# Performance work log

Hardware: AMD Instinct MI355X
Metric: run time of the kernel (lower is better)

Reference implementation:

```python
import jax, jax.numpy as jnp
import numpy as np

B, N, D, H = 4, 2048, 512, 8
HD = D // H


def setup_inputs() -> dict:
    key = jax.random.key(0)
    ks = jax.random.split(key, 12)
    s = 1.0 / np.sqrt(D)
    return {
        "node_feat": jax.random.normal(ks[0], (B, N, D), jnp.float32),
        "edge_weights": jax.random.uniform(ks[1], (B, N, N), jnp.float32),
        "adj_matrix": jax.random.uniform(ks[2], (B, N, N), jnp.float32),
        "masks": jnp.ones((B, N), jnp.float32),
        "class_token": 0.02 * jax.random.normal(ks[3], (1, 1, D), jnp.float32),
        "Wq": jax.random.uniform(ks[4], (D, D), jnp.float32, -s, s),
        "bq": jnp.zeros((D,), jnp.float32),
        "Wk": jax.random.uniform(ks[5], (D, D), jnp.float32, -s, s),
        "bk": jnp.zeros((D,), jnp.float32),
        "Wv": jax.random.uniform(ks[6], (D, D), jnp.float32, -s, s),
        "bv": jnp.zeros((D,), jnp.float32),
        "Wo": jax.random.uniform(ks[7], (D, D), jnp.float32, -s, s),
        "bo": jnp.zeros((D,), jnp.float32),
        "gamma": jnp.ones((D,), jnp.float32),
        "beta": jnp.zeros((D,), jnp.float32),
    }


def _attn_mask(edge_weights, masks):
    # inner block: edge gates + self-loops, clamped at 1
    inner = jnp.minimum(edge_weights + jnp.eye(N, dtype=edge_weights.dtype), 1.0)
    top = jnp.concatenate([jnp.ones((B, 1, 1), edge_weights.dtype), masks[:, None, :]], axis=2)  # [B,1,1+N]
    bot = jnp.concatenate([jnp.ones((B, N, 1), edge_weights.dtype), inner], axis=2)              # [B,N,1+N]
    m = jnp.concatenate([top, bot], axis=1)  # [B,1+N,1+N]
    ext = jnp.concatenate([jnp.ones((B, 1), masks.dtype), masks], axis=1)  # [B,1+N], CLS always valid
    return m * ext[:, None, :] * ext[:, :, None]


def reference(node_feat, edge_weights, adj_matrix, masks, class_token,
              Wq, bq, Wk, bk, Wv, bv, Wo, bo, gamma, beta):
    x = jnp.concatenate([jnp.broadcast_to(class_token, (B, 1, D)), node_feat], axis=1)  # [B,1+N,D]
    S = 1 + N
    q = (x @ Wq.T + bq).reshape(B, S, H, HD).transpose(0, 2, 1, 3)
    k = (x @ Wk.T + bk).reshape(B, S, H, HD).transpose(0, 2, 1, 3)
    v = (x @ Wv.T + bv).reshape(B, S, H, HD).transpose(0, 2, 1, 3)
    scores = jnp.einsum('bhqd,bhkd->bhqk', q, k) / jnp.sqrt(jnp.float32(HD))
    m = _attn_mask(edge_weights, masks)
    scores = jnp.where(m[:, None, :, :] == 0, jnp.float32(-1e9), scores)
    attn = jax.nn.softmax(scores, axis=-1)
    out = jnp.einsum('bhqk,bhkd->bhqd', attn, v).transpose(0, 2, 1, 3).reshape(B, S, D)
    out = out @ Wo.T + bo
    y = out + x
    mu = jnp.mean(y, axis=-1, keepdims=True)
    var = jnp.mean((y - mu) ** 2, axis=-1, keepdims=True)
    y = (y - mu) / jnp.sqrt(var + 1e-5) * gamma + beta
    return y[:, 0, :]
```

## Files before the change

kernel.cpp:

```cpp
#include <hip/hip_runtime.h>

#define B_ 4
#define N_ 2048
#define D_ 512
#define H_ 8
#define S_ (N_ + 1)
#define NSLOT 132

#define Q0_OFF 0
#define TQ_OFF 1024
#define PW_OFF 8192
#define PZ_OFF (PW_OFF + NSLOT * B_ * H_ * D_)
#define W_OFF  (PZ_OFF + NSLOT * B_ * H_)
#define O0_OFF (W_OFF + B_ * H_ * D_)
#define Y_OFF  (O0_OFF + B_ * D_)

__device__ __forceinline__ float wave_reduce_sum(float v) {
    #pragma unroll
    for (int off = 32; off > 0; off >>= 1) v += __shfl_down(v, off, 64);
    return v;
}
__device__ __forceinline__ float wave_allreduce_sum(float v) {
    #pragma unroll
    for (int off = 1; off < 64; off <<= 1) v += __shfl_xor(v, off, 64);
    return v;
}

__global__ void q0_kernel(const float* __restrict__ ct,
                          const float* __restrict__ Wq, const float* __restrict__ bq,
                          float* __restrict__ ws) {
    int wv = threadIdx.x >> 6, lane = threadIdx.x & 63;
    int r = blockIdx.x * 8 + wv;
    const float4* c4 = (const float4*)ct;
    float4 ca = c4[lane * 2], cb = c4[lane * 2 + 1];
    const float4* row = (const float4*)(Wq + (size_t)r * D_);
    float4 a = row[lane * 2], b = row[lane * 2 + 1];
    float acc = a.x*ca.x + a.y*ca.y + a.z*ca.z + a.w*ca.w
              + b.x*cb.x + b.y*cb.y + b.z*cb.z + b.w*cb.w;
    acc = wave_reduce_sum(acc);
    if (lane == 0) ws[Q0_OFF + r] = acc + bq[r];
}

__global__ void tq_kernel(const float* __restrict__ Wk, float* __restrict__ ws) {
    int h = blockIdx.x, jc = blockIdx.y;
    int tid = threadIdx.x;
    __shared__ float q0s[64];
    if (tid < 64) q0s[tid] = ws[Q0_OFF + h * 64 + tid];
    __syncthreads();
    int j = jc * 128 + tid;
    float acc = 0.f;
    #pragma unroll 8
    for (int d2 = 0; d2 < 64; ++d2)
        acc += q0s[d2] * Wk[(size_t)(h * 64 + d2) * D_ + j];
    ws[TQ_OFF + h * D_ + j] = acc;
}

__global__ void fused_kernel(const float* __restrict__ nf, const float* __restrict__ ct,
                             const float* __restrict__ masks, float* __restrict__ ws) {
    int chunk = blockIdx.x, b = blockIdx.y;
    int wv = threadIdx.x >> 6, lane = threadIdx.x & 63;
    int slot = chunk * 4 + wv;
    int s0 = chunk * 64 + wv * 16;
    const float4* tq4 = (const float4*)(ws + TQ_OFF);
    float4 tqa[H_], tqb[H_];
    #pragma unroll
    for (int h = 0; h < H_; ++h) {
        tqa[h] = tq4[h * 128 + lane * 2];
        tqb[h] = tq4[h * 128 + lane * 2 + 1];
    }
    float4 acca[H_], accb[H_];
    float z[H_];
    #pragma unroll
    for (int h = 0; h < H_; ++h) {
        acca[h] = make_float4(0.f, 0.f, 0.f, 0.f);
        accb[h] = make_float4(0.f, 0.f, 0.f, 0.f);
        z[h] = 0.f;
    }
    for (int i = 0; i < 16; ++i) {
        int s = s0 + i;
        bool valid = (s < S_);
        const float* xrow = (!valid || s == 0) ? ct : (nf + ((size_t)b * N_ + (s - 1)) * D_);
        const float4* x4 = (const float4*)xrow;
        float4 xa = x4[lane * 2], xb = x4[lane * 2 + 1];
        float msk = 1.0f;
        if (valid && s > 0) msk = masks[b * N_ + s - 1];
        float gate = (valid && msk != 0.0f) ? 1.0f : 0.0f;
        float p[H_];
        #pragma unroll
        for (int h = 0; h < H_; ++h) {
            p[h] = tqa[h].x*xa.x + tqa[h].y*xa.y + tqa[h].z*xa.z + tqa[h].w*xa.w
                 + tqb[h].x*xb.x + tqb[h].y*xb.y + tqb[h].z*xb.z + tqb[h].w*xb.w;
            p[h] = wave_allreduce_sum(p[h]);
        }
        #pragma unroll
        for (int h = 0; h < H_; ++h) {
            float e = gate * __expf(p[h] * 0.125f);
            z[h] += e;
            acca[h].x += e * xa.x; acca[h].y += e * xa.y;
            acca[h].z += e * xa.z; acca[h].w += e * xa.w;
            accb[h].x += e * xb.x; accb[h].y += e * xb.y;
            accb[h].z += e * xb.z; accb[h].w += e * xb.w;
        }
    }
    float4* pw4 = (float4*)(ws + PW_OFF);
    size_t base = ((size_t)slot * B_ + b) * H_;
    #pragma unroll
    for (int h = 0; h < H_; ++h) {
        pw4[(base + h) * 128 + lane * 2]     = acca[h];
        pw4[(base + h) * 128 + lane * 2 + 1] = accb[h];
    }
    if (lane == 0) {
        #pragma unroll
        for (int h = 0; h < H_; ++h)
            ws[PZ_OFF + (slot * B_ + b) * H_ + h] = z[h];
    }
}

__global__ void reduce_w_kernel(float* __restrict__ ws) {
    int b = blockIdx.x / H_, h = blockIdx.x % H_;
    int tid = threadIdx.x;
    __shared__ float zl[128];
    float zp = 0.f;
    for (int slot = tid; slot < NSLOT; slot += 128)
        zp += ws[PZ_OFF + (slot * B_ + b) * H_ + h];
    zl[tid] = zp;
    __syncthreads();
    for (int st = 64; st > 0; st >>= 1) {
        if (tid < st) zl[tid] += zl[tid + st];
        __syncthreads();
    }
    float zinv = 1.0f / zl[0];
    const float4* pw4 = (const float4*)(ws + PW_OFF);
    float4 acc = make_float4(0.f, 0.f, 0.f, 0.f);
    #pragma unroll 4
    for (int slot = 0; slot < NSLOT; ++slot) {
        float4 v = pw4[(((size_t)slot * B_ + b) * H_ + h) * 128 + tid];
        acc.x += v.x; acc.y += v.y; acc.z += v.z; acc.w += v.w;
    }
    acc.x *= zinv; acc.y *= zinv; acc.z *= zinv; acc.w *= zinv;
    ((float4*)(ws + W_OFF))[(b * H_ + h) * 128 + tid] = acc;
}

__global__ void wv_kernel(const float* __restrict__ Wv, const float* __restrict__ bv,
                          float* __restrict__ ws) {
    int b = blockIdx.x;
    int wv = threadIdx.x >> 6, lane = threadIdx.x & 63;
    int r = blockIdx.y * 4 + wv;
    const float4* wrow = (const float4*)(ws + W_OFF + (size_t)b * H_ * D_ + (size_t)(r >> 6) * D_);
    float4 wa = wrow[lane * 2], wb = wrow[lane * 2 + 1];
    const float4* row = (const float4*)(Wv + (size_t)r * D_);
    float4 a = row[lane * 2], c = row[lane * 2 + 1];
    float acc = a.x*wa.x + a.y*wa.y + a.z*wa.z + a.w*wa.w
              + c.x*wb.x + c.y*wb.y + c.z*wb.z + c.w*wb.w;
    acc = wave_reduce_sum(acc);
    if (lane == 0) ws[O0_OFF + b * D_ + r] = acc + bv[r];
}

__global__ void wo_kernel(const float* __restrict__ Wo, const float* __restrict__ bo,
                          const float* __restrict__ ct, float* __restrict__ ws) {
    int b = blockIdx.x;
    int wv = threadIdx.x >> 6, lane = threadIdx.x & 63;
    int r = blockIdx.y * 4 + wv;
    const float4* ov = (const float4*)(ws + O0_OFF + (size_t)b * D_);
    float4 oa = ov[lane * 2], ob = ov[lane * 2 + 1];
    const float4* row = (const float4*)(Wo + (size_t)r * D_);
    float4 a = row[lane * 2], c = row[lane * 2 + 1];
    float acc = a.x*oa.x + a.y*oa.y + a.z*oa.z + a.w*oa.w
              + c.x*ob.x + c.y*ob.y + c.z*ob.z + c.w*ob.w;
    acc = wave_reduce_sum(acc);
    if (lane == 0) ws[Y_OFF + b * D_ + r] = acc + bo[r] + ct[r];
}

__global__ void ln_kernel(const float* __restrict__ gamma, const float* __restrict__ beta,
                          const float* __restrict__ ws, float* __restrict__ out) {
    int b = blockIdx.x;
    int tid = threadIdx.x, wv = tid >> 6, lane = tid & 63;
    float v = ws[Y_OFF + b * D_ + tid];
    float s1 = v, s2 = v * v;
    #pragma unroll
    for (int off = 32; off > 0; off >>= 1) {
        s1 += __shfl_down(s1, off, 64);
        s2 += __shfl_down(s2, off, 64);
    }
    __shared__ float r1[8], r2[8];
    if (lane == 0) { r1[wv] = s1; r2[wv] = s2; }
    __syncthreads();
    if (tid == 0) {
        float a = 0.f, c = 0.f;
        for (int i = 0; i < 8; ++i) { a += r1[i]; c += r2[i]; }
        r1[0] = a; r2[0] = c;
    }
    __syncthreads();
    float mean = r1[0] * (1.0f / D_);
    float var  = r2[0] * (1.0f / D_) - mean * mean;
    float rinv = rsqrtf(var + 1e-5f);
    out[b * D_ + tid] = (v - mean) * rinv * gamma[tid] + beta[tid];
}

extern "C" void kernel_launch(void* const* d_in, const int* in_sizes, int n_in,
                              void* d_out, int out_size, void* d_ws, size_t ws_size,
                              hipStream_t stream) {
    const float* nf    = (const float*)d_in[0];
    const float* masks = (const float*)d_in[3];
    const float* ct    = (const float*)d_in[4];
    const float* Wq    = (const float*)d_in[5];
    const float* bq    = (const float*)d_in[6];
    const float* Wk    = (const float*)d_in[7];
    const float* Wv    = (const float*)d_in[9];
    const float* bv    = (const float*)d_in[10];
    const float* Wo    = (const float*)d_in[11];
    const float* bo    = (const float*)d_in[12];
    const float* gamma = (const float*)d_in[13];
    const float* beta  = (const float*)d_in[14];
    float* ws  = (float*)d_ws;
    float* out = (float*)d_out;

    hipLaunchKernelGGL(q0_kernel, dim3(64), dim3(512), 0, stream, ct, Wq, bq, ws);
    hipLaunchKernelGGL(tq_kernel, dim3(H_, 4), dim3(128), 0, stream, Wk, ws);
    hipLaunchKernelGGL(fused_kernel, dim3(33, B_), dim3(256), 0, stream, nf, ct, masks, ws);
    hipLaunchKernelGGL(reduce_w_kernel, dim3(B_ * H_), dim3(128), 0, stream, ws);
    hipLaunchKernelGGL(wv_kernel, dim3(B_, 128), dim3(256), 0, stream, Wv, bv, ws);
    hipLaunchKernelGGL(wo_kernel, dim3(B_, 128), dim3(256), 0, stream, Wo, bo, ct, ws);
    hipLaunchKernelGGL(ln_kernel, dim3(B_), dim3(512), 0, stream, gamma, beta, ws, out);
}
```

Baseline: 233.5 us.

## Split fused attention pass into separate score and weighted-sum kernels

The single fused kernel, which computed scores, exponentials and the weighted sum of rows per wave over 16 rows, is replaced by two kernels. A scores kernel gives each row its own wave and writes the gated exponentials to workspace. A wsum kernel then accumulates weighted node features over 32-row chunks using the scores held in shared memory. The goal is far more blocks, to fill the GPU and cut the long serial shuffle chains per wave. The cost is reading the node features twice, plus an extra launch and a workspace round trip for the scores; the reduce kernel is also given a wider grid.

After: 190.3 us (median of 2 runs). 1.23x faster.

```diff
diff --git a/kernel.cpp b/kernel.cpp
--- a/kernel.cpp
+++ b/kernel.cpp
@@ -5,15 +5,17 @@
 #define D_ 512
 #define H_ 8
 #define S_ (N_ + 1)
-#define NSLOT 132
-
-#define Q0_OFF 0
-#define TQ_OFF 1024
-#define PW_OFF 8192
-#define PZ_OFF (PW_OFF + NSLOT * B_ * H_ * D_)
-#define W_OFF  (PZ_OFF + NSLOT * B_ * H_)
-#define O0_OFF (W_OFF + B_ * H_ * D_)
-#define Y_OFF  (O0_OFF + B_ * D_)
+#define SC 32
+#define NCH 65
+
+#define Q0_OFF   0
+#define TQ_OFF   1024
+#define ATTN_OFF 8192
+#define PW_OFF   81920
+#define PZ_OFF   (PW_OFF + NCH * B_ * H_ * D_)
+#define W_OFF    (PZ_OFF + NCH * B_ * H_ + 32)
+#define O0_OFF   (W_OFF + B_ * H_ * D_)
+#define Y_OFF    (O0_OFF + B_ * D_)
 
 __device__ __forceinline__ float wave_reduce_sum(float v) {
     #pragma unroll
@@ -55,90 +57,82 @@
     ws[TQ_OFF + h * D_ + j] = acc;
 }
 
-__global__ void fused_kernel(const float* __restrict__ nf, const float* __restrict__ ct,
-                             const float* __restrict__ masks, float* __restrict__ ws) {
-    int chunk = blockIdx.x, b = blockIdx.y;
-    int wv = threadIdx.x >> 6, lane = threadIdx.x & 63;
-    int slot = chunk * 4 + wv;
-    int s0 = chunk * 64 + wv * 16;
-    const float4* tq4 = (const float4*)(ws + TQ_OFF);
-    float4 tqa[H_], tqb[H_];
+__global__ void __launch_bounds__(512)
+scores_kernel(const float* __restrict__ nf, const float* __restrict__ ct,
+              const float* __restrict__ masks, float* __restrict__ ws) {
+    int b = blockIdx.y;
+    int wv = threadIdx.x >> 6, lane = threadIdx.x & 63;
+    int s = blockIdx.x * 8 + wv;
+    if (s >= S_) return;
+    const float* xrow = (s == 0) ? ct : (nf + ((size_t)b * N_ + (s - 1)) * D_);
+    const float4* x4 = (const float4*)xrow;
+    float4 xa = x4[lane];
+    float4 xb = x4[64 + lane];
+    float gate = 1.0f;
+    if (s > 0) gate = (masks[b * N_ + s - 1] != 0.0f) ? 1.0f : 0.0f;
+    const float4* t4 = (const float4*)(ws + TQ_OFF);
+    float p[H_];
     #pragma unroll
     for (int h = 0; h < H_; ++h) {
-        tqa[h] = tq4[h * 128 + lane * 2];
-        tqb[h] = tq4[h * 128 + lane * 2 + 1];
-    }
-    float4 acca[H_], accb[H_];
-    float z[H_];
-    #pragma unroll
-    for (int h = 0; h < H_; ++h) {
-        acca[h] = make_float4(0.f, 0.f, 0.f, 0.f);
-        accb[h] = make_float4(0.f, 0.f, 0.f, 0.f);
-        z[h] = 0.f;
-    }
-    for (int i = 0; i < 16; ++i) {
-        int s = s0 + i;
-        bool valid = (s < S_);
-        const float* xrow = (!valid || s == 0) ? ct : (nf + ((size_t)b * N_ + (s - 1)) * D_);
-        const float4* x4 = (const float4*)xrow;
-        float4 xa = x4[lane * 2], xb = x4[lane * 2 + 1];
-        float msk = 1.0f;
-        if (valid && s > 0) msk = masks[b * N_ + s - 1];
-        float gate = (valid && msk != 0.0f) ? 1.0f : 0.0f;
-        float p[H_];
-        #pragma unroll
-        for (int h = 0; h < H_; ++h) {
-            p[h] = tqa[h].x*xa.x + tqa[h].y*xa.y + tqa[h].z*xa.z + tqa[h].w*xa.w
-                 + tqb[h].x*xb.x + tqb[h].y*xb.y + tqb[h].z*xb.z + tqb[h].w*xb.w;
-            p[h] = wave_allreduce_sum(p[h]);
-        }
-        #pragma unroll
-        for (int h = 0; h < H_; ++h) {
-            float e = gate * __expf(p[h] * 0.125f);
-            z[h] += e;
-            acca[h].x += e * xa.x; acca[h].y += e * xa.y;
-            acca[h].z += e * xa.z; acca[h].w += e * xa.w;
-            accb[h].x += e * xb.x; accb[h].y += e * xb.y;
-            accb[h].z += e * xb.z; accb[h].w += e * xb.w;
-        }
-    }
-    float4* pw4 = (float4*)(ws + PW_OFF);
-    size_t base = ((size_t)slot * B_ + b) * H_;
-    #pragma unroll
-    for (int h = 0; h < H_; ++h) {
-        pw4[(base + h) * 128 + lane * 2]     = acca[h];
-        pw4[(base + h) * 128 + lane * 2 + 1] = accb[h];
+        float4 ta = t4[h * 128 + lane], tb = t4[h * 128 + 64 + lane];
+        p[h] = ta.x*xa.x + ta.y*xa.y + ta.z*xa.z + ta.w*xa.w
+             + tb.x*xb.x + tb.y*xb.y + tb.z*xb.z + tb.w*xb.w;
+        p[h] = wave_allreduce_sum(p[h]);
     }
     if (lane == 0) {
         #pragma unroll
         for (int h = 0; h < H_; ++h)
-            ws[PZ_OFF + (slot * B_ + b) * H_ + h] = z[h];
+            ws[ATTN_OFF + (size_t)(b * H_ + h) * S_ + s] = gate * __expf(p[h] * 0.125f);
+    }
+}
+
+__global__ void __launch_bounds__(512)
+wsum_kernel(const float* __restrict__ nf, const float* __restrict__ ct,
+            float* __restrict__ ws) {
+    int chunk = blockIdx.x, b = blockIdx.y;
+    int tid = threadIdx.x;
+    __shared__ float sa[H_][SC];
+    int s0 = chunk * SC;
+    if (tid < H_ * SC) {
+        int h = tid >> 5, ss = tid & 31;
+        int s = s0 + ss;
+        sa[h][ss] = (s < S_) ? ws[ATTN_OFF + (size_t)(b * H_ + h) * S_ + s] : 0.f;
+    }
+    __syncthreads();
+    float acc[H_];
+    #pragma unroll
+    for (int h = 0; h < H_; ++h) acc[h] = 0.f;
+    int smax = min(SC, S_ - s0);
+    for (int ss = 0; ss < smax; ++ss) {
+        int s = s0 + ss;
+        const float* xrow = (s == 0) ? ct : (nf + ((size_t)b * N_ + (s - 1)) * D_);
+        float xv = xrow[tid];
+        #pragma unroll
+        for (int h = 0; h < H_; ++h) acc[h] += sa[h][ss] * xv;
+    }
+    size_t base = ((size_t)chunk * B_ + b) * H_;
+    #pragma unroll
+    for (int h = 0; h < H_; ++h)
+        ws[PW_OFF + (base + h) * D_ + tid] = acc[h];
+    if (tid < H_) {
+        float z = 0.f;
+        #pragma unroll 8
+        for (int ss = 0; ss < SC; ++ss) z += sa[tid][ss];
+        ws[PZ_OFF + base + tid] = z;
     }
 }
 
 __global__ void reduce_w_kernel(float* __restrict__ ws) {
-    int b = blockIdx.x / H_, h = blockIdx.x % H_;
-    int tid = threadIdx.x;
-    __shared__ float zl[128];
-    float zp = 0.f;
-    for (int slot = tid; slot < NSLOT; slot += 128)
-        zp += ws[PZ_OFF + (slot * B_ + b) * H_ + h];
-    zl[tid] = zp;
-    __syncthreads();
-    for (int st = 64; st > 0; st >>= 1) {
-        if (tid < st) zl[tid] += zl[tid + st];
-        __syncthreads();
-    }
-    float zinv = 1.0f / zl[0];
-    const float4* pw4 = (const float4*)(ws + PW_OFF);
-    float4 acc = make_float4(0.f, 0.f, 0.f, 0.f);
-    #pragma unroll 4
-    for (int slot = 0; slot < NSLOT; ++slot) {
-        float4 v = pw4[(((size_t)slot * B_ + b) * H_ + h) * 128 + tid];
-        acc.x += v.x; acc.y += v.y; acc.z += v.z; acc.w += v.w;
-    }
-    acc.x *= zinv; acc.y *= zinv; acc.z *= zinv; acc.w *= zinv;
-    ((float4*)(ws + W_OFF))[(b * H_ + h) * 128 + tid] = acc;
+    int bh = blockIdx.x;
+    int j = blockIdx.y * 128 + threadIdx.x;
+    float z = 0.f;
+    #pragma unroll 5
+    for (int c = 0; c < NCH; ++c) z += ws[PZ_OFF + (size_t)(c * B_ * H_) + bh];
+    float acc = 0.f;
+    #pragma unroll 5
+    for (int c = 0; c < NCH; ++c)
+        acc += ws[PW_OFF + ((size_t)(c * B_ * H_) + bh) * D_ + j];
+    ws[W_OFF + (size_t)bh * D_ + j] = acc / z;
 }
 
 __global__ void wv_kernel(const float* __restrict__ Wv, const float* __restrict__ bv,
@@ -217,8 +211,9 @@
 
     hipLaunchKernelGGL(q0_kernel, dim3(64), dim3(512), 0, stream, ct, Wq, bq, ws);
     hipLaunchKernelGGL(tq_kernel, dim3(H_, 4), dim3(128), 0, stream, Wk, ws);
-    hipLaunchKernelGGL(fused_kernel, dim3(33, B_), dim3(256), 0, stream, nf, ct, masks, ws);
-    hipLaunchKernelGGL(reduce_w_kernel, dim3(B_ * H_), dim3(128), 0, stream, ws);
+    hipLaunchKernelGGL(scores_kernel, dim3(257, B_), dim3(512), 0, stream, nf, ct, masks, ws);
+    hipLaunchKernelGGL(wsum_kernel, dim3(NCH, B_), dim3(512), 0, stream, nf, ct, ws);
+    hipLaunchKernelGGL(reduce_w_kernel, dim3(B_ * H_, 4), dim3(128), 0, stream, ws);
     hipLaunchKernelGGL(wv_kernel, dim3(B_, 128), dim3(256), 0, stream, Wv, bv, ws);
     hipLaunchKernelGGL(wo_kernel, dim3(B_, 128), dim3(256), 0, stream, Wo, bo, ct, ws);
     hipLaunchKernelGGL(ln_kernel, dim3(B_), dim3(512), 0, stream, gamma, beta, ws, out);
```
